# Performance work log

Hardware: AMD Instinct MI355X
Metric: run time of the kernel (lower is better)

The kernel has to match this reference:

```python
import jax, jax.numpy as jnp
import numpy as np

N_NODES = 50000
N_EDGES = 800000
IN_CH = 128
HID = 32
HEADS = 4
OUT_CH = 64
N_GRAPHS = 64


def setup_inputs() -> dict:
    key = jax.random.key(0)
    ks = jax.random.split(key, 16)
    x = jax.random.normal(ks[0], (N_NODES, IN_CH), dtype=jnp.float32)
    edge_index = jax.random.randint(ks[1], (2, N_EDGES), 0, N_NODES, dtype=jnp.int64)
    edge_attr = jax.random.normal(ks[2], (N_EDGES, 8), dtype=jnp.float32)
    nodeIDs = jnp.sort(jax.random.randint(ks[3], (N_NODES,), 0, N_GRAPHS, dtype=jnp.int64))
    s = 0.1
    W1 = jax.random.normal(ks[4], (IN_CH, HEADS * HID), dtype=jnp.float32) * s
    att_src1 = jax.random.normal(ks[5], (HEADS, HID), dtype=jnp.float32) * s
    att_dst1 = jax.random.normal(ks[6], (HEADS, HID), dtype=jnp.float32) * s
    b1 = jax.random.normal(ks[7], (HEADS * HID,), dtype=jnp.float32) * s
    W2 = jax.random.normal(ks[8], (HEADS * HID, 16), dtype=jnp.float32) * s
    att_src2 = jax.random.normal(ks[9], (1, 16), dtype=jnp.float32) * s
    att_dst2 = jax.random.normal(ks[10], (1, 16), dtype=jnp.float32) * s
    b2 = jax.random.normal(ks[11], (16,), dtype=jnp.float32) * s
    Wf = jax.random.normal(ks[12], (16, OUT_CH), dtype=jnp.float32) * s
    bf = jax.random.normal(ks[13], (OUT_CH,), dtype=jnp.float32) * s
    return dict(x=x, edge_index=edge_index, edge_attr=edge_attr, nodeIDs=nodeIDs,
                W1=W1, att_src1=att_src1, att_dst1=att_dst1, b1=b1,
                W2=W2, att_src2=att_src2, att_dst2=att_dst2, b2=b2,
                Wf=Wf, bf=bf)


def gat_conv(x, src, dst, n, W, a_src, a_dst, b, heads, out_ch, concat):
    # linear transform -> [N, H, C]
    h = (x @ W).reshape(n, heads, out_ch)
    # per-node attention logits [N, H]
    asrc = jnp.sum(h * a_src, axis=-1)
    adst = jnp.sum(h * a_dst, axis=-1)
    e = jax.nn.leaky_relu(asrc[src] + adst[dst], 0.2)  # [E, H]
    # segment softmax over edges sharing the same destination node
    m = jax.ops.segment_max(e, dst, num_segments=n)
    e = jnp.exp(e - m[dst])
    s = jax.ops.segment_sum(e, dst, num_segments=n)
    alpha = e / (s[dst] + 1e-16)
    # weighted scatter-add aggregation: [N, H, C]
    out = jax.ops.segment_sum(alpha[:, :, None] * h[src], dst, num_segments=n)
    out = out.reshape(n, heads * out_ch) if concat else out.mean(axis=1)
    return out + b


def reference(x, edge_index, edge_attr, nodeIDs, W1, att_src1, att_dst1, b1,
              W2, att_src2, att_dst2, b2, Wf, bf):
    n = x.shape[0]
    # GATConv default: add self-loops
    loop = jnp.arange(n, dtype=edge_index.dtype)
    src = jnp.concatenate([edge_index[0], loop])
    dst = jnp.concatenate([edge_index[1], loop])
    # eval mode: dropout is identity. edge_attr ignored (no edge_dim in GATConv).
    h = jax.nn.relu(gat_conv(x, src, dst, n, W1, att_src1, att_dst1, b1, HEADS, HID, True))
    h = jax.nn.relu(gat_conv(h, src, dst, n, W2, att_src2, att_dst2, b2, 1, 16, False))
    # global mean pool over graphs
    sums = jax.ops.segment_sum(h, nodeIDs, num_segments=N_GRAPHS)
    cnts = jax.ops.segment_sum(jnp.ones((n,), dtype=h.dtype), nodeIDs, num_segments=N_GRAPHS)
    pooled = sums / jnp.maximum(cnts, 1.0)[:, None]  # [G, 16]
    return pooled @ Wf + bf
```

## Files before the change

kernel.cpp:

```cpp
#include <hip/hip_runtime.h>
#include <hip/hip_bf16.h>


__device__ __forceinline__ float lrelu02(float x) { return x > 0.f ? x : 0.2f * x; }

__device__ __forceinline__ unsigned short f2bf(float f) {
    unsigned b = __float_as_uint(f);
    return (unsigned short)((b + 0x7fffu + ((b >> 16) & 1u)) >> 16);
}
__device__ __forceinline__ float bf_lo(unsigned u) { return __uint_as_float(u << 16); }
__device__ __forceinline__ float bf_hi(unsigned u) { return __uint_as_float(u & 0xffff0000u); }

__global__ __launch_bounds__(256) void k_gemm1h(
    const float* __restrict__ x, const float* __restrict__ W1,
    const float* __restrict__ a_src, const float* __restrict__ a_dst,
    unsigned short* __restrict__ H1b, float* __restrict__ asrcv, float* __restrict__ adstv, int N,
    const int* __restrict__ dst, int* __restrict__ deg, int E, int GB)
{
    if ((int)blockIdx.x >= GB) {
        const int nb = gridDim.x - GB;
        const int bi = blockIdx.x - GB;
        for (int i = bi * 256 + threadIdx.x; i < E; i += nb * 256)
            atomicAdd(&deg[dst[i]], 1);
        return;
    }

    __shared__ float sA[32][68];
    __shared__ float sB[32][128];
    const int tid = threadIdx.x;
    const int m0 = (tid >> 5) * 8;
    const int n0 = (tid & 31) * 4;
    const int rowbase = blockIdx.x * 64;

    float acc[8][4];
#pragma unroll
    for (int i = 0; i < 8; ++i)
#pragma unroll
        for (int j = 0; j < 4; ++j) acc[i][j] = 0.f;

    const int am  = tid >> 2;
    const int ak0 = (tid & 3) * 8;
    const int bk  = tid >> 3;
    const int bn0 = (tid & 7) * 16;

    for (int kt = 0; kt < 128; kt += 32) {
        int grow = rowbase + am;
        const float* xp = x + (size_t)(grow < N ? grow : N - 1) * 128 + kt + ak0;
        float4 xa = *(const float4*)(xp);
        float4 xb = *(const float4*)(xp + 4);
        sA[ak0 + 0][am] = xa.x; sA[ak0 + 1][am] = xa.y;
        sA[ak0 + 2][am] = xa.z; sA[ak0 + 3][am] = xa.w;
        sA[ak0 + 4][am] = xb.x; sA[ak0 + 5][am] = xb.y;
        sA[ak0 + 6][am] = xb.z; sA[ak0 + 7][am] = xb.w;
        const float* wp = W1 + (size_t)(kt + bk) * 128 + bn0;
#pragma unroll
        for (int q = 0; q < 4; ++q)
            *(float4*)&sB[bk][bn0 + q * 4] = *(const float4*)(wp + q * 4);
        __syncthreads();
#pragma unroll
        for (int k = 0; k < 32; ++k) {
            float4 a0 = *(const float4*)&sA[k][m0];
            float4 a1 = *(const float4*)&sA[k][m0 + 4];
            float4 b  = *(const float4*)&sB[k][n0];
            float av[8] = {a0.x, a0.y, a0.z, a0.w, a1.x, a1.y, a1.z, a1.w};
            float bv[4] = {b.x, b.y, b.z, b.w};
#pragma unroll
            for (int i = 0; i < 8; ++i)
#pragma unroll
                for (int j = 0; j < 4; ++j)
                    acc[i][j] = fmaf(av[i], bv[j], acc[i][j]);
        }
        __syncthreads();
    }

    const int h = n0 >> 5;
    const float4 asv = *(const float4*)&a_src[n0];
    const float4 adv = *(const float4*)&a_dst[n0];
#pragma unroll
    for (int i = 0; i < 8; ++i) {
        int grow = rowbase + m0 + i;
        if (grow < N) {
            uint2 p;
            p.x = (unsigned)f2bf(acc[i][0]) | ((unsigned)f2bf(acc[i][1]) << 16);
            p.y = (unsigned)f2bf(acc[i][2]) | ((unsigned)f2bf(acc[i][3]) << 16);
            *(uint2*)&H1b[(size_t)grow * 128 + n0] = p;
        }
        float vs = acc[i][0]*asv.x + acc[i][1]*asv.y + acc[i][2]*asv.z + acc[i][3]*asv.w;
        float vd = acc[i][0]*adv.x + acc[i][1]*adv.y + acc[i][2]*adv.z + acc[i][3]*adv.w;
        vs += __shfl_xor(vs, 1); vd += __shfl_xor(vd, 1);
        vs += __shfl_xor(vs, 2); vd += __shfl_xor(vd, 2);
        vs += __shfl_xor(vs, 4); vd += __shfl_xor(vd, 4);
        if ((tid & 7) == 0 && grow < N) {
            asrcv[grow * 4 + h] = vs;
            adstv[grow * 4 + h] = vd;
        }
    }
}

__global__ __launch_bounds__(256) void k_gemm2(
    const float* __restrict__ X, const float* __restrict__ b1,
    const float* __restrict__ W2, const float* __restrict__ a_src2, const float* __restrict__ a_dst2,
    unsigned short* __restrict__ H2b, float* __restrict__ asrcv, float* __restrict__ adstv, int N)
{
    __shared__ float xs[64][132];
    __shared__ float ws[128][16];
    const int tid = threadIdx.x;
    const int rowbase = blockIdx.x * 64;
    {
        int k = tid >> 1, c0 = (tid & 1) * 8;
        *(float4*)&ws[k][c0]     = *(const float4*)&W2[k * 16 + c0];
        *(float4*)&ws[k][c0 + 4] = *(const float4*)&W2[k * 16 + c0 + 4];
    }
    {
        int r = tid >> 2, k0 = (tid & 3) * 32;
        int grow = rowbase + r;
        const float* xp = X + (size_t)(grow < N ? grow : N - 1) * 128 + k0;
#pragma unroll
        for (int q = 0; q < 8; ++q) {
            float4 v  = *(const float4*)(xp + q * 4);
            float4 bb = *(const float4*)&b1[k0 + q * 4];
            xs[r][k0 + q*4 + 0] = fmaxf(v.x + bb.x, 0.f);
            xs[r][k0 + q*4 + 1] = fmaxf(v.y + bb.y, 0.f);
            xs[r][k0 + q*4 + 2] = fmaxf(v.z + bb.z, 0.f);
            xs[r][k0 + q*4 + 3] = fmaxf(v.w + bb.w, 0.f);
        }
    }
    __syncthreads();
    const int r = tid >> 2, c0 = (tid & 3) * 4;
    float acc[4] = {0.f, 0.f, 0.f, 0.f};
#pragma unroll 16
    for (int k = 0; k < 128; ++k) {
        float xv = xs[r][k];
        float4 w = *(const float4*)&ws[k][c0];
        acc[0] = fmaf(xv, w.x, acc[0]);
        acc[1] = fmaf(xv, w.y, acc[1]);
        acc[2] = fmaf(xv, w.z, acc[2]);
        acc[3] = fmaf(xv, w.w, acc[3]);
    }
    int grow = rowbase + r;
    const float4 as4 = *(const float4*)&a_src2[c0];
    const float4 ad4 = *(const float4*)&a_dst2[c0];
    float vs = acc[0]*as4.x + acc[1]*as4.y + acc[2]*as4.z + acc[3]*as4.w;
    float vd = acc[0]*ad4.x + acc[1]*ad4.y + acc[2]*ad4.z + acc[3]*ad4.w;
    vs += __shfl_xor(vs, 1); vd += __shfl_xor(vd, 1);
    vs += __shfl_xor(vs, 2); vd += __shfl_xor(vd, 2);
    if (grow < N) {
        uint2 p;
        p.x = (unsigned)f2bf(acc[0]) | ((unsigned)f2bf(acc[1]) << 16);
        p.y = (unsigned)f2bf(acc[2]) | ((unsigned)f2bf(acc[3]) << 16);
        *(uint2*)&H2b[(size_t)grow * 16 + c0] = p;
        if ((tid & 3) == 0) { asrcv[grow] = vs; adstv[grow] = vd; }
    }
}

__global__ __launch_bounds__(1024) void k_s1(
    const int* __restrict__ deg, int* __restrict__ scn, int* __restrict__ bsum, int N)
{
    __shared__ int wsum[16];
    const int lane = threadIdx.x & 63, w = threadIdx.x >> 6;
    const int i = blockIdx.x * 1024 + threadIdx.x;
    int v = (i < N) ? deg[i] : 0;
    int sc = v;
#pragma unroll
    for (int s = 1; s < 64; s <<= 1) {
        int t = __shfl_up(sc, s);
        if (lane >= s) sc += t;
    }
    if (lane == 63) wsum[w] = sc;
    __syncthreads();
    if (threadIdx.x < 16) {
        int t = wsum[threadIdx.x];
#pragma unroll
        for (int s = 1; s < 16; s <<= 1) {
            int u = __shfl_up(t, s);
            if ((int)threadIdx.x >= s) t += u;
        }
        wsum[threadIdx.x] = t;
    }
    __syncthreads();
    int incl = ((w == 0) ? 0 : wsum[w - 1]) + sc;
    if (i < N) scn[i] = incl;
    if (threadIdx.x == 1023) bsum[blockIdx.x] = incl;
}

__global__ __launch_bounds__(64) void k_s2(
    const int* __restrict__ bsum, int* __restrict__ bpre, int nb)
{
    int t = threadIdx.x;
    int v = (t < nb) ? bsum[t] : 0;
    int sc = v;
#pragma unroll
    for (int s = 1; s < 64; s <<= 1) {
        int u = __shfl_up(sc, s);
        if (t >= s) sc += u;
    }
    if (t < nb) bpre[t] = sc - v;
}

__global__ __launch_bounds__(1024) void k_s3(
    const int* __restrict__ deg, const int* __restrict__ scn, const int* __restrict__ bpre,
    int* __restrict__ off, int* __restrict__ cur, int N)
{
    const int i = blockIdx.x * 1024 + threadIdx.x;
    if (i == 0) off[0] = 0;
    if (i < N) {
        int incl = bpre[blockIdx.x] + scn[i];
        off[i + 1] = incl;
        cur[i] = incl - deg[i];
    }
}

__global__ __launch_bounds__(256) void k_scatterx(
    const int* __restrict__ src, const int* __restrict__ dst,
    int* __restrict__ cur, unsigned short* __restrict__ ecsr, int E, int N)
{
    const int g  = blockIdx.x & 7;
    const int lo = (int)(((long long)N * g) >> 3);
    const int hi = (int)(((long long)N * (g + 1)) >> 3);
    const int nb = gridDim.x >> 3;
    const int bi = blockIdx.x >> 3;
    for (int i = bi * 256 + threadIdx.x; i < E; i += nb * 256) {
        int d = dst[i];
        if (d >= lo && d < hi) {
            int p = atomicAdd(&cur[d], 1);
            ecsr[p] = (unsigned short)src[i];
        }
    }
}

__global__ __launch_bounds__(256) void k_agg1(
    const unsigned short* __restrict__ H1b, const float* __restrict__ asrc, const float* __restrict__ adst,
    const int* __restrict__ off, const unsigned short* __restrict__ ecsr,
    float* __restrict__ out, int N)
{
    __shared__ float sEs[4][64 * 4];
    __shared__ int   sSs[4][64];
    const int w = threadIdx.x >> 6, lane = threadIdx.x & 63;
    float* sE = sEs[w];
    int*   sS = sSs[w];
    const int n = blockIdx.x * 4 + w;
    if (n >= N) return;
    const int beg = off[n], deg = off[n + 1] - beg;

    const float4 ad4 = *(const float4*)&adst[n * 4];
    const float4 as4 = *(const float4*)&asrc[n * 4];
    float es0 = __expf(lrelu02(as4.x + ad4.x));
    float es1 = __expf(lrelu02(as4.y + ad4.y));
    float es2 = __expf(lrelu02(as4.z + ad4.z));
    float es3 = __expf(lrelu02(as4.w + ad4.w));
    float ssum0 = es0, ssum1 = es1, ssum2 = es2, ssum3 = es3;
    if (lane != 0) { ssum0 = 0.f; ssum1 = 0.f; ssum2 = 0.f; ssum3 = 0.f; }

    const int g = lane >> 4, q = lane & 15;
    const int c0 = q * 8, h = q >> 2;
    float acc[8] = {0.f,0.f,0.f,0.f,0.f,0.f,0.f,0.f};

    for (int cb = 0; cb < deg; cb += 64) {
        int cnt = min(64, deg - cb);
        if (lane < cnt) {
            int s = (int)ecsr[beg + cb + lane];
            sS[lane] = s;
            const float4 a = *(const float4*)&asrc[s * 4];
            float e0 = __expf(lrelu02(a.x + ad4.x));
            float e1 = __expf(lrelu02(a.y + ad4.y));
            float e2 = __expf(lrelu02(a.z + ad4.z));
            float e3 = __expf(lrelu02(a.w + ad4.w));
            ssum0 += e0; ssum1 += e1; ssum2 += e2; ssum3 += e3;
            sE[lane * 4 + 0] = e0; sE[lane * 4 + 1] = e1;
            sE[lane * 4 + 2] = e2; sE[lane * 4 + 3] = e3;
        }
        for (int j = g; j < cnt; j += 4) {
            int s = sS[j];
            float e = sE[j * 4 + h];
            uint4 u = *(const uint4*)&H1b[(size_t)s * 128 + c0];
            acc[0] = fmaf(e, bf_lo(u.x), acc[0]);
            acc[1] = fmaf(e, bf_hi(u.x), acc[1]);
            acc[2] = fmaf(e, bf_lo(u.y), acc[2]);
            acc[3] = fmaf(e, bf_hi(u.y), acc[3]);
            acc[4] = fmaf(e, bf_lo(u.z), acc[4]);
            acc[5] = fmaf(e, bf_hi(u.z), acc[5]);
            acc[6] = fmaf(e, bf_lo(u.w), acc[6]);
            acc[7] = fmaf(e, bf_hi(u.w), acc[7]);
        }
    }

#pragma unroll
    for (int xm = 32; xm >= 1; xm >>= 1) {
        ssum0 += __shfl_xor(ssum0, xm);
        ssum1 += __shfl_xor(ssum1, xm);
        ssum2 += __shfl_xor(ssum2, xm);
        ssum3 += __shfl_xor(ssum3, xm);
    }
#pragma unroll
    for (int k = 0; k < 8; ++k) {
        acc[k] += __shfl_xor(acc[k], 16);
        acc[k] += __shfl_xor(acc[k], 32);
    }
    if (g == 0) {
        float ssv = (h == 0) ? ssum0 : (h == 1) ? ssum1 : (h == 2) ? ssum2 : ssum3;
        float esv = (h == 0) ? es0   : (h == 1) ? es1   : (h == 2) ? es2   : es3;
        float inv = 1.f / (ssv + 1e-16f);
        uint4 u = *(const uint4*)&H1b[(size_t)n * 128 + c0];
        float o[8];
        o[0] = (acc[0] + esv * bf_lo(u.x)) * inv;
        o[1] = (acc[1] + esv * bf_hi(u.x)) * inv;
        o[2] = (acc[2] + esv * bf_lo(u.y)) * inv;
        o[3] = (acc[3] + esv * bf_hi(u.y)) * inv;
        o[4] = (acc[4] + esv * bf_lo(u.z)) * inv;
        o[5] = (acc[5] + esv * bf_hi(u.z)) * inv;
        o[6] = (acc[6] + esv * bf_lo(u.w)) * inv;
        o[7] = (acc[7] + esv * bf_hi(u.w)) * inv;
        *(float4*)&out[(size_t)n * 128 + c0]     = make_float4(o[0], o[1], o[2], o[3]);
        *(float4*)&out[(size_t)n * 128 + c0 + 4] = make_float4(o[4], o[5], o[6], o[7]);
    }
}

__global__ __launch_bounds__(256) void k_agg2(
    const unsigned short* __restrict__ H2b, const float* __restrict__ asrc, const float* __restrict__ adst,
    const int* __restrict__ off, const unsigned short* __restrict__ ecsr,
    float* __restrict__ out, int N)
{
    __shared__ float sEs[4][64];
    __shared__ int   sSs[4][64];
    const int w = threadIdx.x >> 6, lane = threadIdx.x & 63;
    float* sE = sEs[w];
    int*   sS = sSs[w];
    const int n = blockIdx.x * 4 + w;
    if (n >= N) return;
    const int beg = off[n], deg = off[n + 1] - beg;

    const float adv = adst[n];
    float eself = __expf(lrelu02(asrc[n] + adv));
    float ssum = (lane == 0) ? eself : 0.f;

    const int g = lane >> 3, q = lane & 7;
    const int c0 = q * 2;
    float acc0 = 0.f, acc1 = 0.f;

    for (int cb = 0; cb < deg; cb += 64) {
        int cnt = min(64, deg - cb);
        if (lane < cnt) {
            int s = (int)ecsr[beg + cb + lane];
            sS[lane] = s;
            float e = __expf(lrelu02(asrc[s] + adv));
            ssum += e;
            sE[lane] = e;
        }
        for (int j = g; j < cnt; j += 8) {
            int s = sS[j];
            float e = sE[j];
            unsigned u = *(const unsigned*)&H2b[(size_t)s * 16 + c0];
            acc0 = fmaf(e, bf_lo(u), acc0);
            acc1 = fmaf(e, bf_hi(u), acc1);
        }
    }
#pragma unroll
    for (int xm = 32; xm >= 1; xm >>= 1) ssum += __shfl_xor(ssum, xm);
    acc0 += __shfl_xor(acc0, 8);  acc1 += __shfl_xor(acc1, 8);
    acc0 += __shfl_xor(acc0, 16); acc1 += __shfl_xor(acc1, 16);
    acc0 += __shfl_xor(acc0, 32); acc1 += __shfl_xor(acc1, 32);
    if (g == 0) {
        float inv = 1.f / (ssum + 1e-16f);
        unsigned u = *(const unsigned*)&H2b[(size_t)n * 16 + c0];
        float2 o;
        o.x = (acc0 + eself * bf_lo(u)) * inv;
        o.y = (acc1 + eself * bf_hi(u)) * inv;
        *(float2*)&out[(size_t)n * 16 + c0] = o;
    }
}

__global__ __launch_bounds__(256) void k_poolfinal(
    const float* __restrict__ out2, const float* __restrict__ b2,
    const int* __restrict__ nodeIDs, const float* __restrict__ Wf,
    const float* __restrict__ bf, float* __restrict__ outp, int N)
{
    int g = blockIdx.x;
    int lo = 0, hi = N;
    while (lo < hi) { int mid = (lo + hi) >> 1; if (nodeIDs[mid] < g) lo = mid + 1; else hi = mid; }
    int start = lo;
    lo = 0; hi = N;
    while (lo < hi) { int mid = (lo + hi) >> 1; if (nodeIDs[mid] < g + 1) lo = mid + 1; else hi = mid; }
    int end = lo;

    int c = threadIdx.x & 15, grp = threadIdx.x >> 4;
    float bc = b2[c];
    float acc = 0.f;
    for (int n = start + grp; n < end; n += 16)
        acc += fmaxf(out2[(size_t)n * 16 + c] + bc, 0.f);

    __shared__ float sd[256];
    __shared__ float p16[16];
    sd[threadIdx.x] = acc;
    __syncthreads();
#pragma unroll
    for (int s = 8; s >= 1; s >>= 1) {
        if (grp < s) sd[threadIdx.x] += sd[(grp + s) * 16 + c];
        __syncthreads();
    }
    if (threadIdx.x < 16) {
        float cnt = (float)(end - start);
        p16[threadIdx.x] = sd[threadIdx.x] / fmaxf(cnt, 1.f);
    }
    __syncthreads();
    if (threadIdx.x < 64) {
        int o = threadIdx.x;
        float a = bf[o];
#pragma unroll
        for (int k = 0; k < 16; ++k)
            a = fmaf(p16[k], Wf[k * 64 + o], a);
        outp[(size_t)g * 64 + o] = a;
    }
}

extern "C" void kernel_launch(void* const* d_in, const int* in_sizes, int n_in,
                              void* d_out, int out_size, void* d_ws, size_t ws_size,
                              hipStream_t stream)
{
    const float* x   = (const float*)d_in[0];
    const int*   ei  = (const int*)  d_in[1];
    const int*   nid = (const int*)  d_in[3];
    const float* W1  = (const float*)d_in[4];
    const float* as1 = (const float*)d_in[5];
    const float* ad1 = (const float*)d_in[6];
    const float* b1  = (const float*)d_in[7];
    const float* W2  = (const float*)d_in[8];
    const float* as2 = (const float*)d_in[9];
    const float* ad2 = (const float*)d_in[10];
    const float* b2  = (const float*)d_in[11];
    const float* Wf  = (const float*)d_in[12];
    const float* bf  = (const float*)d_in[13];
    float* outp = (float*)d_out;

    const int N = in_sizes[0] / 128;
    const int E = in_sizes[1] / 2;
    const int* src = ei;
    const int* dst = ei + E;

    char* ws = (char*)d_ws;
    size_t off_b = 0;
    auto alloc = [&](size_t bytes) -> char* {
        char* p = ws + off_b;
        off_b += (bytes + 255) & ~(size_t)255;
        return p;
    };

    unsigned short* H1b  = (unsigned short*)alloc((size_t)N * 128 * 2);
    unsigned short* H2b  = (unsigned short*)alloc((size_t)N * 16 * 2);
    unsigned short* ecsr = (unsigned short*)alloc((size_t)E * 2);
    float* out1   = (float*)alloc((size_t)N * 128 * 4);
    float* asrc1  = (float*)alloc((size_t)N * 4 * 4);
    float* adst1  = (float*)alloc((size_t)N * 4 * 4);
    float* out2   = (float*)alloc((size_t)N * 16 * 4);
    float* asrc2  = (float*)alloc((size_t)N * 4);
    float* adst2  = (float*)alloc((size_t)N * 4);
    int*   deg    = (int*)  alloc((size_t)N * 4);
    int*   cur    = (int*)  alloc((size_t)N * 4);
    int*   offp   = (int*)  alloc((size_t)(N + 1) * 4);
    int*   scn    = (int*)  alloc((size_t)N * 4);
    int*   bsum   = (int*)  alloc((size_t)64 * 4);
    int*   bpre   = (int*)  alloc((size_t)64 * 4);

    auto cdiv = [](long long a, long long b) { return (int)((a + b - 1) / b); };

    const int GB = cdiv(N, 64);
    const int NB = cdiv(N, 1024);

    hipMemsetAsync(deg, 0, (size_t)N * 4, stream);

    k_gemm1h<<<GB + 256, 256, 0, stream>>>(x, W1, as1, ad1, H1b, asrc1, adst1, N,
                                           dst, deg, E, GB);
    k_s1<<<NB, 1024, 0, stream>>>(deg, scn, bsum, N);
    k_s2<<<1, 64, 0, stream>>>(bsum, bpre, NB);
    k_s3<<<NB, 1024, 0, stream>>>(deg, scn, bpre, offp, cur, N);
    k_scatterx<<<1024, 256, 0, stream>>>(src, dst, cur, ecsr, E, N);

    k_agg1<<<cdiv(N, 4), 256, 0, stream>>>(H1b, asrc1, adst1, offp, ecsr, out1, N);

    k_gemm2<<<cdiv(N, 64), 256, 0, stream>>>(out1, b1, W2, as2, ad2, H2b, asrc2, adst2, N);
    k_agg2<<<cdiv(N, 4), 256, 0, stream>>>(H2b, asrc2, adst2, offp, ecsr, out2, N);

    k_poolfinal<<<out_size / 64, 256, 0, stream>>>(out2, b2, nid, Wf, bf, outp, N);
}
```

Before: 183.6 us.

## Use bf16 MFMA for layer-1 GEMM and split aggregation by head

The layer-1 projection moves from a scalar FP32 FMA tile loop to bf16 MFMA 16x16x32 instructions. W1 is pre-transposed and converted to bf16 by a small prep kernel, x is converted to bf16 in shared memory, and the output is staged through LDS for coalesced stores. The layer-1 aggregation is restructured so each block handles one head over a grid-stride set of nodes, which shrinks per-edge work and keeps a head's feature slice contiguous. Rounding x to bf16 adds some precision loss, and each edge's source index and logits are now read four times, once per head.

```diff
diff --git a/kernel.cpp b/kernel.cpp
--- a/kernel.cpp
+++ b/kernel.cpp
@@ -11,8 +11,18 @@
 __device__ __forceinline__ float bf_lo(unsigned u) { return __uint_as_float(u << 16); }
 __device__ __forceinline__ float bf_hi(unsigned u) { return __uint_as_float(u & 0xffff0000u); }
 
+typedef __attribute__((ext_vector_type(8))) short short8v;
+typedef __attribute__((ext_vector_type(4))) float f32x4;
+
+__global__ __launch_bounds__(128) void k_prep(
+    const float* __restrict__ W1, unsigned short* __restrict__ W1tb)
+{
+    int n = blockIdx.x, k = threadIdx.x;
+    W1tb[n * 128 + k] = f2bf(W1[k * 128 + n]);
+}
+
 __global__ __launch_bounds__(256) void k_gemm1h(
-    const float* __restrict__ x, const float* __restrict__ W1,
+    const float* __restrict__ x, const unsigned short* __restrict__ W1tb,
     const float* __restrict__ a_src, const float* __restrict__ a_dst,
     unsigned short* __restrict__ H1b, float* __restrict__ asrcv, float* __restrict__ adstv, int N,
     const int* __restrict__ dst, int* __restrict__ deg, int E, int GB)
@@ -25,74 +35,91 @@
         return;
     }
 
-    __shared__ float sA[32][68];
-    __shared__ float sB[32][128];
+    __shared__ unsigned short sX[64][136];
+    __shared__ unsigned short sW[128][136];
     const int tid = threadIdx.x;
-    const int m0 = (tid >> 5) * 8;
-    const int n0 = (tid & 31) * 4;
     const int rowbase = blockIdx.x * 64;
 
-    float acc[8][4];
-#pragma unroll
-    for (int i = 0; i < 8; ++i)
-#pragma unroll
-        for (int j = 0; j < 4; ++j) acc[i][j] = 0.f;
-
-    const int am  = tid >> 2;
-    const int ak0 = (tid & 3) * 8;
-    const int bk  = tid >> 3;
-    const int bn0 = (tid & 7) * 16;
-
-    for (int kt = 0; kt < 128; kt += 32) {
-        int grow = rowbase + am;
-        const float* xp = x + (size_t)(grow < N ? grow : N - 1) * 128 + kt + ak0;
-        float4 xa = *(const float4*)(xp);
-        float4 xb = *(const float4*)(xp + 4);
-        sA[ak0 + 0][am] = xa.x; sA[ak0 + 1][am] = xa.y;
-        sA[ak0 + 2][am] = xa.z; sA[ak0 + 3][am] = xa.w;
-        sA[ak0 + 4][am] = xb.x; sA[ak0 + 5][am] = xb.y;
-        sA[ak0 + 6][am] = xb.z; sA[ak0 + 7][am] = xb.w;
-        const float* wp = W1 + (size_t)(kt + bk) * 128 + bn0;
-#pragma unroll
-        for (int q = 0; q < 4; ++q)
-            *(float4*)&sB[bk][bn0 + q * 4] = *(const float4*)(wp + q * 4);
-        __syncthreads();
-#pragma unroll
-        for (int k = 0; k < 32; ++k) {
-            float4 a0 = *(const float4*)&sA[k][m0];
-            float4 a1 = *(const float4*)&sA[k][m0 + 4];
-            float4 b  = *(const float4*)&sB[k][n0];
-            float av[8] = {a0.x, a0.y, a0.z, a0.w, a1.x, a1.y, a1.z, a1.w};
-            float bv[4] = {b.x, b.y, b.z, b.w};
-#pragma unroll
-            for (int i = 0; i < 8; ++i)
-#pragma unroll
-                for (int j = 0; j < 4; ++j)
-                    acc[i][j] = fmaf(av[i], bv[j], acc[i][j]);
-        }
-        __syncthreads();
-    }
-
-    const int h = n0 >> 5;
-    const float4 asv = *(const float4*)&a_src[n0];
-    const float4 adv = *(const float4*)&a_dst[n0];
-#pragma unroll
-    for (int i = 0; i < 8; ++i) {
-        int grow = rowbase + m0 + i;
+    {
+        int r = tid >> 2, k0 = (tid & 3) * 32;
+        int grow = rowbase + r;
+        const float* xp = x + (size_t)(grow < N ? grow : N - 1) * 128 + k0;
+        unsigned* sp = (unsigned*)&sX[r][k0];
+#pragma unroll
+        for (int q = 0; q < 8; ++q) {
+            float4 v = *(const float4*)(xp + q * 4);
+            sp[q * 2 + 0] = (unsigned)f2bf(v.x) | ((unsigned)f2bf(v.y) << 16);
+            sp[q * 2 + 1] = (unsigned)f2bf(v.z) | ((unsigned)f2bf(v.w) << 16);
+        }
+    }
+    {
+        int n = tid >> 1, k0 = (tid & 1) * 64;
+        const uint4* wp = (const uint4*)(W1tb + n * 128 + k0);
+#pragma unroll
+        for (int q = 0; q < 8; ++q)
+            *(uint4*)&sW[n][k0 + q * 8] = wp[q];
+    }
+    __syncthreads();
+
+    const int w  = tid >> 6, l = tid & 63;
+    const int m0 = w * 16;
+    const int mr = l & 15, kg = l >> 4;
+
+    f32x4 acc[8];
+#pragma unroll
+    for (int nt = 0; nt < 8; ++nt) acc[nt] = (f32x4){0.f, 0.f, 0.f, 0.f};
+
+#pragma unroll
+    for (int kk = 0; kk < 4; ++kk) {
+        const int kbase = kk * 32 + kg * 8;
+        short8v a = *(const short8v*)&sX[m0 + mr][kbase];
+#pragma unroll
+        for (int nt = 0; nt < 8; ++nt) {
+            short8v b = *(const short8v*)&sW[nt * 16 + mr][kbase];
+            acc[nt] = __builtin_amdgcn_mfma_f32_16x16x32_bf16(a, b, acc[nt], 0, 0, 0);
+        }
+    }
+
+    {
+        float as_[8], ad_[8];
+#pragma unroll
+        for (int nt = 0; nt < 8; ++nt) { as_[nt] = a_src[nt * 16 + mr]; ad_[nt] = a_dst[nt * 16 + mr]; }
+#pragma unroll
+        for (int j = 0; j < 4; ++j) {
+            float vs[4], vd[4];
+#pragma unroll
+            for (int h = 0; h < 4; ++h) {
+                vs[h] = acc[2 * h][j] * as_[2 * h] + acc[2 * h + 1][j] * as_[2 * h + 1];
+                vd[h] = acc[2 * h][j] * ad_[2 * h] + acc[2 * h + 1][j] * ad_[2 * h + 1];
+#pragma unroll
+                for (int xm = 1; xm <= 8; xm <<= 1) {
+                    vs[h] += __shfl_xor(vs[h], xm);
+                    vd[h] += __shfl_xor(vd[h], xm);
+                }
+            }
+            int grow = rowbase + m0 + kg * 4 + j;
+            if (mr == 0 && grow < N) {
+                *(float4*)&asrcv[grow * 4] = make_float4(vs[0], vs[1], vs[2], vs[3]);
+                *(float4*)&adstv[grow * 4] = make_float4(vd[0], vd[1], vd[2], vd[3]);
+            }
+        }
+    }
+
+    __syncthreads();
+#pragma unroll
+    for (int nt = 0; nt < 8; ++nt)
+#pragma unroll
+        for (int j = 0; j < 4; ++j)
+            sX[m0 + kg * 4 + j][nt * 16 + mr] = f2bf(acc[nt][j]);
+    __syncthreads();
+    {
+        int r = tid >> 2, k0 = (tid & 3) * 32;
+        int grow = rowbase + r;
         if (grow < N) {
-            uint2 p;
-            p.x = (unsigned)f2bf(acc[i][0]) | ((unsigned)f2bf(acc[i][1]) << 16);
-            p.y = (unsigned)f2bf(acc[i][2]) | ((unsigned)f2bf(acc[i][3]) << 16);
-            *(uint2*)&H1b[(size_t)grow * 128 + n0] = p;
-        }
-        float vs = acc[i][0]*asv.x + acc[i][1]*asv.y + acc[i][2]*asv.z + acc[i][3]*asv.w;
-        float vd = acc[i][0]*adv.x + acc[i][1]*adv.y + acc[i][2]*adv.z + acc[i][3]*adv.w;
-        vs += __shfl_xor(vs, 1); vd += __shfl_xor(vd, 1);
-        vs += __shfl_xor(vs, 2); vd += __shfl_xor(vd, 2);
-        vs += __shfl_xor(vs, 4); vd += __shfl_xor(vd, 4);
-        if ((tid & 7) == 0 && grow < N) {
-            asrcv[grow * 4 + h] = vs;
-            adstv[grow * 4 + h] = vd;
+            const uint4* sp = (const uint4*)&sX[r][k0];
+            uint4* dp = (uint4*)&H1b[(size_t)grow * 128 + k0];
+#pragma unroll
+            for (int q = 0; q < 4; ++q) dp[q] = sp[q];
         }
     }
 }
@@ -228,90 +255,76 @@
     }
 }
 
-__global__ __launch_bounds__(256) void k_agg1(
+__global__ __launch_bounds__(256) void k_agg1h(
     const unsigned short* __restrict__ H1b, const float* __restrict__ asrc, const float* __restrict__ adst,
     const int* __restrict__ off, const unsigned short* __restrict__ ecsr,
     float* __restrict__ out, int N)
 {
-    __shared__ float sEs[4][64 * 4];
+    __shared__ float sEs[4][64];
     __shared__ int   sSs[4][64];
+    const int h  = blockIdx.x & 3;
+    const int bi = blockIdx.x >> 2;
+    const int nb = gridDim.x >> 2;
     const int w = threadIdx.x >> 6, lane = threadIdx.x & 63;
     float* sE = sEs[w];
     int*   sS = sSs[w];
-    const int n = blockIdx.x * 4 + w;
-    if (n >= N) return;
-    const int beg = off[n], deg = off[n + 1] - beg;
-
-    const float4 ad4 = *(const float4*)&adst[n * 4];
-    const float4 as4 = *(const float4*)&asrc[n * 4];
-    float es0 = __expf(lrelu02(as4.x + ad4.x));
-    float es1 = __expf(lrelu02(as4.y + ad4.y));
-    float es2 = __expf(lrelu02(as4.z + ad4.z));
-    float es3 = __expf(lrelu02(as4.w + ad4.w));
-    float ssum0 = es0, ssum1 = es1, ssum2 = es2, ssum3 = es3;
-    if (lane != 0) { ssum0 = 0.f; ssum1 = 0.f; ssum2 = 0.f; ssum3 = 0.f; }
-
-    const int g = lane >> 4, q = lane & 15;
-    const int c0 = q * 8, h = q >> 2;
-    float acc[8] = {0.f,0.f,0.f,0.f,0.f,0.f,0.f,0.f};
-
-    for (int cb = 0; cb < deg; cb += 64) {
-        int cnt = min(64, deg - cb);
-        if (lane < cnt) {
-            int s = (int)ecsr[beg + cb + lane];
-            sS[lane] = s;
-            const float4 a = *(const float4*)&asrc[s * 4];
-            float e0 = __expf(lrelu02(a.x + ad4.x));
-            float e1 = __expf(lrelu02(a.y + ad4.y));
-            float e2 = __expf(lrelu02(a.z + ad4.z));
-            float e3 = __expf(lrelu02(a.w + ad4.w));
-            ssum0 += e0; ssum1 += e1; ssum2 += e2; ssum3 += e3;
-            sE[lane * 4 + 0] = e0; sE[lane * 4 + 1] = e1;
-            sE[lane * 4 + 2] = e2; sE[lane * 4 + 3] = e3;
-        }
-        for (int j = g; j < cnt; j += 4) {
-            int s = sS[j];
-            float e = sE[j * 4 + h];
-            uint4 u = *(const uint4*)&H1b[(size_t)s * 128 + c0];
-            acc[0] = fmaf(e, bf_lo(u.x), acc[0]);
-            acc[1] = fmaf(e, bf_hi(u.x), acc[1]);
-            acc[2] = fmaf(e, bf_lo(u.y), acc[2]);
-            acc[3] = fmaf(e, bf_hi(u.y), acc[3]);
-            acc[4] = fmaf(e, bf_lo(u.z), acc[4]);
-            acc[5] = fmaf(e, bf_hi(u.z), acc[5]);
-            acc[6] = fmaf(e, bf_lo(u.w), acc[6]);
-            acc[7] = fmaf(e, bf_hi(u.w), acc[7]);
-        }
-    }
-
-#pragma unroll
-    for (int xm = 32; xm >= 1; xm >>= 1) {
-        ssum0 += __shfl_xor(ssum0, xm);
-        ssum1 += __shfl_xor(ssum1, xm);
-        ssum2 += __shfl_xor(ssum2, xm);
-        ssum3 += __shfl_xor(ssum3, xm);
-    }
-#pragma unroll
-    for (int k = 0; k < 8; ++k) {
-        acc[k] += __shfl_xor(acc[k], 16);
-        acc[k] += __shfl_xor(acc[k], 32);
-    }
-    if (g == 0) {
-        float ssv = (h == 0) ? ssum0 : (h == 1) ? ssum1 : (h == 2) ? ssum2 : ssum3;
-        float esv = (h == 0) ? es0   : (h == 1) ? es1   : (h == 2) ? es2   : es3;
-        float inv = 1.f / (ssv + 1e-16f);
-        uint4 u = *(const uint4*)&H1b[(size_t)n * 128 + c0];
-        float o[8];
-        o[0] = (acc[0] + esv * bf_lo(u.x)) * inv;
-        o[1] = (acc[1] + esv * bf_hi(u.x)) * inv;
-        o[2] = (acc[2] + esv * bf_lo(u.y)) * inv;
-        o[3] = (acc[3] + esv * bf_hi(u.y)) * inv;
-        o[4] = (acc[4] + esv * bf_lo(u.z)) * inv;
-        o[5] = (acc[5] + esv * bf_hi(u.z)) * inv;
-        o[6] = (acc[6] + esv * bf_lo(u.w)) * inv;
-        o[7] = (acc[7] + esv * bf_hi(u.w)) * inv;
-        *(float4*)&out[(size_t)n * 128 + c0]     = make_float4(o[0], o[1], o[2], o[3]);
-        *(float4*)&out[(size_t)n * 128 + c0 + 4] = make_float4(o[4], o[5], o[6], o[7]);
+    const int eg = lane >> 2, cl = lane & 3;
+    const int c0 = h * 32 + cl * 8;
+
+    for (int n = bi * 4 + w; n < N; n += nb * 4) {
+        const int beg = off[n], deg = off[n + 1] - beg;
+        const float adv = adst[n * 4 + h];
+        const float eself = __expf(lrelu02(asrc[n * 4 + h] + adv));
+        float ssum = (lane == 0) ? eself : 0.f;
+        float acc[8] = {0.f,0.f,0.f,0.f,0.f,0.f,0.f,0.f};
+
+        for (int cb = 0; cb < deg; cb += 64) {
+            int cnt = min(64, deg - cb);
+            if (lane < cnt) {
+                int s = (int)ecsr[beg + cb + lane];
+                sS[lane] = s;
+                float e = __expf(lrelu02(asrc[s * 4 + h] + adv));
+                ssum += e;
+                sE[lane] = e;
+            }
+            for (int j = eg; j < cnt; j += 16) {
+                int s = sS[j];
+                float e = sE[j];
+                uint4 u = *(const uint4*)&H1b[(size_t)s * 128 + c0];
+                acc[0] = fmaf(e, bf_lo(u.x), acc[0]);
+                acc[1] = fmaf(e, bf_hi(u.x), acc[1]);
+                acc[2] = fmaf(e, bf_lo(u.y), acc[2]);
+                acc[3] = fmaf(e, bf_hi(u.y), acc[3]);
+                acc[4] = fmaf(e, bf_lo(u.z), acc[4]);
+                acc[5] = fmaf(e, bf_hi(u.z), acc[5]);
+                acc[6] = fmaf(e, bf_lo(u.w), acc[6]);
+                acc[7] = fmaf(e, bf_hi(u.w), acc[7]);
+            }
+        }
+#pragma unroll
+        for (int xm = 32; xm >= 1; xm >>= 1) ssum += __shfl_xor(ssum, xm);
+#pragma unroll
+        for (int k = 0; k < 8; ++k) {
+            acc[k] += __shfl_xor(acc[k], 4);
+            acc[k] += __shfl_xor(acc[k], 8);
+            acc[k] += __shfl_xor(acc[k], 16);
+            acc[k] += __shfl_xor(acc[k], 32);
+        }
+        if (eg == 0) {
+            float inv = 1.f / (ssum + 1e-16f);
+            uint4 u = *(const uint4*)&H1b[(size_t)n * 128 + c0];
+            float o[8];
+            o[0] = (acc[0] + eself * bf_lo(u.x)) * inv;
+            o[1] = (acc[1] + eself * bf_hi(u.x)) * inv;
+            o[2] = (acc[2] + eself * bf_lo(u.y)) * inv;
+            o[3] = (acc[3] + eself * bf_hi(u.y)) * inv;
+            o[4] = (acc[4] + eself * bf_lo(u.z)) * inv;
+            o[5] = (acc[5] + eself * bf_hi(u.z)) * inv;
+            o[6] = (acc[6] + eself * bf_lo(u.w)) * inv;
+            o[7] = (acc[7] + eself * bf_hi(u.w)) * inv;
+            *(float4*)&out[(size_t)n * 128 + c0]     = make_float4(o[0], o[1], o[2], o[3]);
+            *(float4*)&out[(size_t)n * 128 + c0 + 4] = make_float4(o[4], o[5], o[6], o[7]);
+        }
     }
 }
 
@@ -447,6 +460,7 @@
     unsigned short* H1b  = (unsigned short*)alloc((size_t)N * 128 * 2);
     unsigned short* H2b  = (unsigned short*)alloc((size_t)N * 16 * 2);
     unsigned short* ecsr = (unsigned short*)alloc((size_t)E * 2);
+    unsigned short* W1tb = (unsigned short*)alloc((size_t)128 * 128 * 2);
     float* out1   = (float*)alloc((size_t)N * 128 * 4);
     float* asrc1  = (float*)alloc((size_t)N * 4 * 4);
     float* adst1  = (float*)alloc((size_t)N * 4 * 4);
@@ -466,15 +480,16 @@
     const int NB = cdiv(N, 1024);
 
     hipMemsetAsync(deg, 0, (size_t)N * 4, stream);
-
-    k_gemm1h<<<GB + 256, 256, 0, stream>>>(x, W1, as1, ad1, H1b, asrc1, adst1, N,
+    k_prep<<<128, 128, 0, stream>>>(W1, W1tb);
+
+    k_gemm1h<<<GB + 256, 256, 0, stream>>>(x, W1tb, as1, ad1, H1b, asrc1, adst1, N,
                                            dst, deg, E, GB);
     k_s1<<<NB, 1024, 0, stream>>>(deg, scn, bsum, N);
     k_s2<<<1, 64, 0, stream>>>(bsum, bpre, NB);
     k_s3<<<NB, 1024, 0, stream>>>(deg, scn, bpre, offp, cur, N);
     k_scatterx<<<1024, 256, 0, stream>>>(src, dst, cur, ecsr, E, N);
 
-    k_agg1<<<cdiv(N, 4), 256, 0, stream>>>(H1b, asrc1, adst1, offp, ecsr, out1, N);
+    k_agg1h<<<8192, 256, 0, stream>>>(H1b, asrc1, adst1, offp, ecsr, out1, N);
 
     k_gemm2<<<cdiv(N, 64), 256, 0, stream>>>(out1, b1, W2, as2, ad2, H2b, asrc2, adst2, N);
     k_agg2<<<cdiv(N, 4), 256, 0, stream>>>(H2b, asrc2, adst2, offp, ecsr, out2, N);
```

Measured after the change: 246.4 us. 1.34x slower.

## Use bf16 MFMA for first-layer GEMM with pre-transposed bf16 weights

Applied to the files above, without the earlier changes.

Replaces the FP32 shared-memory tiled SIMT GEMM for x@W1 with the 16x16x32 bf16 MFMA instruction. Each wave computes 16 rows directly from registers. A new small kernel transposes W1 to bf16 once per call. Results are staged through LDS so H1 can be written with coalesced 16-byte stores. The attention logits are reduced with wider shuffles and stored as float4. This lowers the GEMM's FP32 FMA cost, but x and W1 are now rounded to bf16 and one extra kernel launch is added.

```diff
diff --git a/kernel.cpp b/kernel.cpp
--- a/kernel.cpp
+++ b/kernel.cpp
@@ -11,8 +11,18 @@
 __device__ __forceinline__ float bf_lo(unsigned u) { return __uint_as_float(u << 16); }
 __device__ __forceinline__ float bf_hi(unsigned u) { return __uint_as_float(u & 0xffff0000u); }
 
+typedef __attribute__((ext_vector_type(8))) short short8v;
+typedef __attribute__((ext_vector_type(4))) float f32x4;
+
+__global__ __launch_bounds__(128) void k_prep(
+    const float* __restrict__ W1, unsigned short* __restrict__ W1tb)
+{
+    int n = blockIdx.x, k = threadIdx.x;
+    W1tb[n * 128 + k] = f2bf(W1[k * 128 + n]);
+}
+
 __global__ __launch_bounds__(256) void k_gemm1h(
-    const float* __restrict__ x, const float* __restrict__ W1,
+    const float* __restrict__ x, const unsigned short* __restrict__ W1tb,
     const float* __restrict__ a_src, const float* __restrict__ a_dst,
     unsigned short* __restrict__ H1b, float* __restrict__ asrcv, float* __restrict__ adstv, int N,
     const int* __restrict__ dst, int* __restrict__ deg, int E, int GB)
@@ -25,74 +35,76 @@
         return;
     }
 
-    __shared__ float sA[32][68];
-    __shared__ float sB[32][128];
+    __shared__ unsigned short sL[4][16][136];
     const int tid = threadIdx.x;
-    const int m0 = (tid >> 5) * 8;
-    const int n0 = (tid & 31) * 4;
+    const int w  = tid >> 6, l = tid & 63;
+    const int mr = l & 15, kg = l >> 4;
+    const int m0 = w * 16;
     const int rowbase = blockIdx.x * 64;
 
-    float acc[8][4];
-#pragma unroll
-    for (int i = 0; i < 8; ++i)
-#pragma unroll
-        for (int j = 0; j < 4; ++j) acc[i][j] = 0.f;
-
-    const int am  = tid >> 2;
-    const int ak0 = (tid & 3) * 8;
-    const int bk  = tid >> 3;
-    const int bn0 = (tid & 7) * 16;
-
-    for (int kt = 0; kt < 128; kt += 32) {
-        int grow = rowbase + am;
-        const float* xp = x + (size_t)(grow < N ? grow : N - 1) * 128 + kt + ak0;
-        float4 xa = *(const float4*)(xp);
-        float4 xb = *(const float4*)(xp + 4);
-        sA[ak0 + 0][am] = xa.x; sA[ak0 + 1][am] = xa.y;
-        sA[ak0 + 2][am] = xa.z; sA[ak0 + 3][am] = xa.w;
-        sA[ak0 + 4][am] = xb.x; sA[ak0 + 5][am] = xb.y;
-        sA[ak0 + 6][am] = xb.z; sA[ak0 + 7][am] = xb.w;
-        const float* wp = W1 + (size_t)(kt + bk) * 128 + bn0;
-#pragma unroll
-        for (int q = 0; q < 4; ++q)
-            *(float4*)&sB[bk][bn0 + q * 4] = *(const float4*)(wp + q * 4);
-        __syncthreads();
-#pragma unroll
-        for (int k = 0; k < 32; ++k) {
-            float4 a0 = *(const float4*)&sA[k][m0];
-            float4 a1 = *(const float4*)&sA[k][m0 + 4];
-            float4 b  = *(const float4*)&sB[k][n0];
-            float av[8] = {a0.x, a0.y, a0.z, a0.w, a1.x, a1.y, a1.z, a1.w};
-            float bv[4] = {b.x, b.y, b.z, b.w};
-#pragma unroll
-            for (int i = 0; i < 8; ++i)
-#pragma unroll
-                for (int j = 0; j < 4; ++j)
-                    acc[i][j] = fmaf(av[i], bv[j], acc[i][j]);
-        }
-        __syncthreads();
-    }
-
-    const int h = n0 >> 5;
-    const float4 asv = *(const float4*)&a_src[n0];
-    const float4 adv = *(const float4*)&a_dst[n0];
-#pragma unroll
-    for (int i = 0; i < 8; ++i) {
-        int grow = rowbase + m0 + i;
+    const int grow_a = rowbase + m0 + mr;
+    const float* xr = x + (size_t)(grow_a < N ? grow_a : N - 1) * 128;
+
+    f32x4 acc[8];
+#pragma unroll
+    for (int nt = 0; nt < 8; ++nt) acc[nt] = (f32x4){0.f, 0.f, 0.f, 0.f};
+
+#pragma unroll
+    for (int kk = 0; kk < 4; ++kk) {
+        const int kbase = kk * 32 + kg * 8;
+        float4 xa = *(const float4*)(xr + kbase);
+        float4 xb = *(const float4*)(xr + kbase + 4);
+        short8v a;
+        unsigned* ap = (unsigned*)&a;
+        ap[0] = (unsigned)f2bf(xa.x) | ((unsigned)f2bf(xa.y) << 16);
+        ap[1] = (unsigned)f2bf(xa.z) | ((unsigned)f2bf(xa.w) << 16);
+        ap[2] = (unsigned)f2bf(xb.x) | ((unsigned)f2bf(xb.y) << 16);
+        ap[3] = (unsigned)f2bf(xb.z) | ((unsigned)f2bf(xb.w) << 16);
+#pragma unroll
+        for (int nt = 0; nt < 8; ++nt) {
+            short8v b = *(const short8v*)&W1tb[(size_t)(nt * 16 + mr) * 128 + kbase];
+            acc[nt] = __builtin_amdgcn_mfma_f32_16x16x32_bf16(a, b, acc[nt], 0, 0, 0);
+        }
+    }
+
+    {
+        float as_[8], ad_[8];
+#pragma unroll
+        for (int nt = 0; nt < 8; ++nt) { as_[nt] = a_src[nt * 16 + mr]; ad_[nt] = a_dst[nt * 16 + mr]; }
+#pragma unroll
+        for (int j = 0; j < 4; ++j) {
+            float vs[4], vd[4];
+#pragma unroll
+            for (int h = 0; h < 4; ++h) {
+                vs[h] = acc[2 * h][j] * as_[2 * h] + acc[2 * h + 1][j] * as_[2 * h + 1];
+                vd[h] = acc[2 * h][j] * ad_[2 * h] + acc[2 * h + 1][j] * ad_[2 * h + 1];
+#pragma unroll
+                for (int xm = 1; xm <= 8; xm <<= 1) {
+                    vs[h] += __shfl_xor(vs[h], xm);
+                    vd[h] += __shfl_xor(vd[h], xm);
+                }
+            }
+            int grow = rowbase + m0 + kg * 4 + j;
+            if (mr == 0 && grow < N) {
+                *(float4*)&asrcv[grow * 4] = make_float4(vs[0], vs[1], vs[2], vs[3]);
+                *(float4*)&adstv[grow * 4] = make_float4(vd[0], vd[1], vd[2], vd[3]);
+            }
+        }
+    }
+
+#pragma unroll
+    for (int nt = 0; nt < 8; ++nt)
+#pragma unroll
+        for (int j = 0; j < 4; ++j)
+            sL[w][kg * 4 + j][nt * 16 + mr] = f2bf(acc[nt][j]);
+    {
+        int r = l >> 2, k0 = (l & 3) * 32;
+        int grow = rowbase + m0 + r;
         if (grow < N) {
-            uint2 p;
-            p.x = (unsigned)f2bf(acc[i][0]) | ((unsigned)f2bf(acc[i][1]) << 16);
-            p.y = (unsigned)f2bf(acc[i][2]) | ((unsigned)f2bf(acc[i][3]) << 16);
-            *(uint2*)&H1b[(size_t)grow * 128 + n0] = p;
-        }
-        float vs = acc[i][0]*asv.x + acc[i][1]*asv.y + acc[i][2]*asv.z + acc[i][3]*asv.w;
-        float vd = acc[i][0]*adv.x + acc[i][1]*adv.y + acc[i][2]*adv.z + acc[i][3]*adv.w;
-        vs += __shfl_xor(vs, 1); vd += __shfl_xor(vd, 1);
-        vs += __shfl_xor(vs, 2); vd += __shfl_xor(vd, 2);
-        vs += __shfl_xor(vs, 4); vd += __shfl_xor(vd, 4);
-        if ((tid & 7) == 0 && grow < N) {
-            asrcv[grow * 4 + h] = vs;
-            adstv[grow * 4 + h] = vd;
+            const uint4* sp = (const uint4*)&sL[w][r][k0];
+            uint4* dp = (uint4*)&H1b[(size_t)grow * 128 + k0];
+#pragma unroll
+            for (int q = 0; q < 4; ++q) dp[q] = sp[q];
         }
     }
 }
@@ -447,6 +459,7 @@
     unsigned short* H1b  = (unsigned short*)alloc((size_t)N * 128 * 2);
     unsigned short* H2b  = (unsigned short*)alloc((size_t)N * 16 * 2);
     unsigned short* ecsr = (unsigned short*)alloc((size_t)E * 2);
+    unsigned short* W1tb = (unsigned short*)alloc((size_t)128 * 128 * 2);
     float* out1   = (float*)alloc((size_t)N * 128 * 4);
     float* asrc1  = (float*)alloc((size_t)N * 4 * 4);
     float* adst1  = (float*)alloc((size_t)N * 4 * 4);
@@ -466,8 +479,9 @@
     const int NB = cdiv(N, 1024);
 
     hipMemsetAsync(deg, 0, (size_t)N * 4, stream);
-
-    k_gemm1h<<<GB + 256, 256, 0, stream>>>(x, W1, as1, ad1, H1b, asrc1, adst1, N,
+    k_prep<<<128, 128, 0, stream>>>(W1, W1tb);
+
+    k_gemm1h<<<GB + 256, 256, 0, stream>>>(x, W1tb, as1, ad1, H1b, asrc1, adst1, N,
                                            dst, deg, E, GB);
     k_s1<<<NB, 1024, 0, stream>>>(deg, scn, bsum, N);
     k_s2<<<1, 64, 0, stream>>>(bsum, bpre, NB);
```

Measured after the change: 193.7 us. +5.5%, slower.
